# Kernel tuning notes

Measured on AMD Instinct MI355X. Metric: run time of the kernel, lower is better.

## Reference

```python
import jax, jax.numpy as jnp
import numpy as np

DIM = 1024
DT_RANK = 64
D_STATE = 16
B, L = 4, 512


def _layer_norm(x, gamma, beta, eps=1e-6):
    mu = jnp.mean(x, axis=-1, keepdims=True)
    var = jnp.mean(jnp.square(x - mu), axis=-1, keepdims=True)
    return (x - mu) * jax.lax.rsqrt(var + eps) * gamma + beta


def _ssm(u, W_x, b_x, W_dt, b_dt, A_log, Dp):
    # u: [b, l, d]  (d = dim_inner)
    r = W_dt.shape[0]
    n = A_log.shape[1]
    A = -jnp.exp(A_log)                                   # [d, n]
    dbc = u @ W_x + b_x                                   # [b, l, r + 2n]
    delta = jax.nn.softplus(dbc[..., :r] @ W_dt + b_dt)   # [b, l, d]
    Bmat = dbc[..., r:r + n]                              # [b, l, n]
    Cmat = dbc[..., r + n:]                               # [b, l, n]
    dA = jnp.exp(jnp.einsum('bld,dn->bldn', delta, A))    # [b, l, d, n]
    dBu = jnp.einsum('bld,bln,bld->bldn', delta, Bmat, u) # [b, l, d, n]

    def step(h, xs):
        dA_t, dBu_t, C_t = xs
        h = dA_t * h + dBu_t                              # [b, d, n]
        y = jnp.einsum('bdn,bn->bd', h, C_t)
        return h, y

    h0 = jnp.zeros((u.shape[0], u.shape[2], n), u.dtype)
    _, ys = jax.lax.scan(
        step, h0,
        (jnp.swapaxes(dA, 0, 1), jnp.swapaxes(dBu, 0, 1), jnp.swapaxes(Cmat, 0, 1)))
    y = jnp.swapaxes(ys, 0, 1)                            # [b, l, d]
    return y + u * Dp


def setup_inputs() -> dict:
    key = jax.random.key(0)
    ks = jax.random.split(key, 16)
    s = 0.02
    d, r, n = DIM, DT_RANK, D_STATE
    inp = {
        'inputs': jax.random.normal(ks[0], (B, L, d), jnp.float32),
        'gamma': jnp.ones((d,), jnp.float32),
        'beta': jnp.zeros((d,), jnp.float32),
        'W_proj': jax.random.normal(ks[1], (d, d), jnp.float32) * s,
        'b_proj': jnp.zeros((d,), jnp.float32),
        'W_fc': jax.random.normal(ks[2], (d, d), jnp.float32) * s,
        'b_fc': jnp.zeros((d,), jnp.float32),
        'W_bc': jax.random.normal(ks[3], (d, d), jnp.float32) * s,
        'b_bc': jnp.zeros((d,), jnp.float32),
        'W_x1': jax.random.normal(ks[4], (d, r + 2 * n), jnp.float32) * s,
        'b_x1': jnp.zeros((r + 2 * n,), jnp.float32),
        'W_dt1': jax.random.normal(ks[5], (r, d), jnp.float32) * s,
        'b_dt1': jnp.full((d,), -4.0, jnp.float32),
        'A_log1': jnp.log(jnp.broadcast_to(jnp.arange(1, n + 1, dtype=jnp.float32), (d, n))),
        'D1': jnp.ones((d,), jnp.float32),
        'W_x2': jax.random.normal(ks[6], (d, r + 2 * n), jnp.float32) * s,
        'b_x2': jnp.zeros((r + 2 * n,), jnp.float32),
        'W_dt2': jax.random.normal(ks[7], (r, d), jnp.float32) * s,
        'b_dt2': jnp.full((d,), -4.0, jnp.float32),
        'A_log2': jnp.log(jnp.broadcast_to(jnp.arange(1, n + 1, dtype=jnp.float32), (d, n))),
        'D2': jnp.ones((d,), jnp.float32),
    }
    return inp


def reference(inputs, gamma, beta, W_proj, b_proj, W_fc, b_fc, W_bc, b_bc,
              W_x1, b_x1, W_dt1, b_dt1, A_log1, D1,
              W_x2, b_x2, W_dt2, b_dt2, A_log2, D2):
    skip = inputs
    x = _layer_norm(inputs, gamma, beta)
    proj = x @ W_proj + b_proj           # same Dense called twice in original
    z = jax.nn.silu(proj)
    # forward direction: 1x1 conv (== dense) -> softplus -> SSM
    u1 = jax.nn.softplus(proj @ W_fc + b_fc)
    y1 = _ssm(u1, W_x1, b_x1, W_dt1, b_dt1, A_log1, D1)
    # backward direction branch (original does not flip the sequence)
    u2 = jax.nn.softplus(proj @ W_bc + b_bc)
    y2 = _ssm(u2, W_x2, b_x2, W_dt2, b_dt2, A_log2, D2)
    return y1 * z + y2 * z + skip
```

## Files before the change

### kernel.cpp

```cpp
#include <hip/hip_runtime.h>
#include <hip/hip_bf16.h>
#include <math.h>

#define DIM 1024
#define NTOK 2048
#define LSEQ 512
#define NB 4
#define DTR 64
#define DST 16
#define NCH 8
#define TCH 64

typedef unsigned short ushort_t;
typedef __attribute__((ext_vector_type(8))) short bf16x8;
typedef __attribute__((ext_vector_type(4))) float f32x4;

__device__ __forceinline__ float softplus_f(float x) {
    return (x > 20.f) ? x : log1pf(__expf(x));
}
__device__ __forceinline__ ushort_t to_bf16_bits(float f) {
    __hip_bfloat16 h = __float2bfloat16(f);
    return *(ushort_t*)&h;
}
__device__ __forceinline__ float bf16_bits_to_f(ushort_t b) {
    return __uint_as_float(((unsigned int)b) << 16);
}
template<int CTRL>
__device__ __forceinline__ float dpp_add(float x) {
    int xi = __float_as_int(x);
    int yi = __builtin_amdgcn_update_dpp(xi, xi, CTRL, 0xF, 0xF, false);
    return x + __int_as_float(yi);
}

__global__ __launch_bounds__(256) void wconv_kernel(
    const float* __restrict__ W0, const float* __restrict__ W1, const float* __restrict__ W2,
    ushort_t* __restrict__ T0, ushort_t* __restrict__ T1, ushort_t* __restrict__ T2) {
    const float* W = blockIdx.z == 0 ? W0 : blockIdx.z == 1 ? W1 : W2;
    ushort_t* T    = blockIdx.z == 0 ? T0 : blockIdx.z == 1 ? T1 : T2;
    __shared__ float tile[64][65];
    const int k0 = blockIdx.x * 64, n0 = blockIdx.y * 64;
    const int tid = threadIdx.x;
    #pragma unroll
    for (int p = 0; p < 16; ++p) {
        int idx = p * 256 + tid;
        int i = idx >> 6, j = idx & 63;
        tile[i][j] = W[(size_t)(k0 + i) * DIM + n0 + j];
    }
    __syncthreads();
    #pragma unroll
    for (int p = 0; p < 16; ++p) {
        int idx = p * 256 + tid;
        int j = idx >> 6, i = idx & 63;
        T[(size_t)(n0 + j) * DIM + k0 + i] = to_bf16_bits(tile[i][j]);
    }
}

__global__ __launch_bounds__(256) void ln_kernel(
    const float* __restrict__ x, const float* __restrict__ gamma,
    const float* __restrict__ beta, ushort_t* __restrict__ out) {
    const int row = blockIdx.x;
    const int tid = threadIdx.x;
    const float4* xr = (const float4*)(x + (size_t)row * DIM);
    float4 v = xr[tid];
    float s  = v.x + v.y + v.z + v.w;
    float sq = v.x*v.x + v.y*v.y + v.z*v.z + v.w*v.w;
    for (int o = 32; o > 0; o >>= 1) {
        s  += __shfl_down(s, o);
        sq += __shfl_down(sq, o);
    }
    __shared__ float red[8];
    if ((tid & 63) == 0) { red[tid >> 6] = s; red[4 + (tid >> 6)] = sq; }
    __syncthreads();
    float st  = red[0] + red[1] + red[2] + red[3];
    float sqt = red[4] + red[5] + red[6] + red[7];
    float mu = st * (1.f / DIM);
    float var = sqt * (1.f / DIM) - mu * mu;
    float rstd = rsqrtf(var + 1e-6f);
    float4 g = ((const float4*)gamma)[tid];
    float4 bt = ((const float4*)beta)[tid];
    ushort4 ob;
    ob.x = to_bf16_bits((v.x - mu) * rstd * g.x + bt.x);
    ob.y = to_bf16_bits((v.y - mu) * rstd * g.y + bt.y);
    ob.z = to_bf16_bits((v.z - mu) * rstd * g.z + bt.z);
    ob.w = to_bf16_bits((v.w - mu) * rstd * g.w + bt.w);
    ((ushort4*)(out + (size_t)row * DIM))[tid] = ob;
}

template<int ACT>
__global__ __launch_bounds__(256) void mfma_gemm(
    const ushort_t* __restrict__ A, const ushort_t* __restrict__ Bt,
    const float* __restrict__ bias, ushort_t* __restrict__ outb, float* __restrict__ outf) {
    __shared__ __align__(16) ushort_t Asl[2][64 * 64];
    __shared__ __align__(16) ushort_t Bsl[2][64 * 64];
    const int tid = threadIdx.x;
    const int bm = blockIdx.y * 64;
    const int bn = blockIdx.x * 64;
    const int lane = tid & 63;
    const int wid = tid >> 6;
    const int r  = lane & 15;
    const int kg = lane >> 4;
    const int wm = wid >> 1, wn = wid & 1;

    f32x4 acc[2][2] = {};

    auto STAGE = [&](int buf, int k0) {
        #pragma unroll
        for (int q = 0; q < 2; ++q) {
            int c = q * 256 + tid;
            int row = c >> 3;
            int ksl = ((c & 7) ^ (row & 7)) << 3;
            __builtin_amdgcn_global_load_lds(
                (const __attribute__((address_space(1))) void*)(A + (size_t)(bm + row) * DIM + k0 + ksl),
                (__attribute__((address_space(3))) void*)(&Asl[buf][c * 8]), 16, 0, 0);
        }
        #pragma unroll
        for (int q = 0; q < 2; ++q) {
            int c = q * 256 + tid;
            int row = c >> 3;
            int ksl = ((c & 7) ^ (row & 7)) << 3;
            __builtin_amdgcn_global_load_lds(
                (const __attribute__((address_space(1))) void*)(Bt + (size_t)(bn + row) * DIM + k0 + ksl),
                (__attribute__((address_space(3))) void*)(&Bsl[buf][c * 8]), 16, 0, 0);
        }
    };

    STAGE(0, 0);
    __syncthreads();
    int cur = 0;
    for (int t = 0; t < DIM / 64; ++t) {
        if (t + 1 < DIM / 64) STAGE(cur ^ 1, (t + 1) * 64);
        #pragma unroll
        for (int kk = 0; kk < 2; ++kk) {
            const int sw = ((kk * 4 + kg) ^ (r & 7)) << 3;
            bf16x8 af[2], bfr[2];
            #pragma unroll
            for (int mi = 0; mi < 2; ++mi)
                af[mi] = *(const bf16x8*)&Asl[cur][(wm * 32 + mi * 16 + r) * 64 + sw];
            #pragma unroll
            for (int nj = 0; nj < 2; ++nj)
                bfr[nj] = *(const bf16x8*)&Bsl[cur][(wn * 32 + nj * 16 + r) * 64 + sw];
            #pragma unroll
            for (int mi = 0; mi < 2; ++mi)
                #pragma unroll
                for (int nj = 0; nj < 2; ++nj)
                    acc[mi][nj] = __builtin_amdgcn_mfma_f32_16x16x32_bf16(af[mi], bfr[nj], acc[mi][nj], 0, 0, 0);
        }
        __syncthreads();
        cur ^= 1;
    }

    #pragma unroll
    for (int nj = 0; nj < 2; ++nj) {
        const int col = bn + wn * 32 + nj * 16 + r;
        const float bv = bias[col];
        #pragma unroll
        for (int mi = 0; mi < 2; ++mi) {
            const int rowb = bm + wm * 32 + mi * 16 + kg * 4;
            #pragma unroll
            for (int j = 0; j < 4; ++j) {
                float v = acc[mi][nj][j] + bv;
                size_t idx = (size_t)(rowb + j) * DIM + col;
                if (ACT == 0) {
                    outb[idx] = to_bf16_bits(v);
                    outf[idx] = v / (1.f + __expf(-v));
                } else {
                    outf[idx] = softplus_f(v);
                }
            }
        }
    }
}

__global__ __launch_bounds__(256) void dbc_kernel(
    const float* __restrict__ u1, const float* __restrict__ u2,
    const float* __restrict__ Wx1, const float* __restrict__ bx1,
    const float* __restrict__ Wx2, const float* __restrict__ bx2,
    float* __restrict__ dbc1, float* __restrict__ dbc2) {
    const int s = blockIdx.y;
    const float* __restrict__ u   = s ? u2   : u1;
    const float* __restrict__ Wx  = s ? Wx2  : Wx1;
    const float* __restrict__ bx  = s ? bx2  : bx1;
    float* __restrict__ dbc       = s ? dbc2 : dbc1;
    const int row0 = blockIdx.x * 8;
    const int tid = threadIdx.x;
    const int kh = tid >> 7;
    const int j  = tid & 127;
    __shared__ float part[8][96];
    float acc[8];
    if (j < 96) {
        const float bj = (kh == 0) ? bx[j] : 0.f;
        #pragma unroll
        for (int r = 0; r < 8; ++r) acc[r] = bj;
        const float* ur = u + (size_t)row0 * DIM + kh * 512;
        const float* wp = Wx + (size_t)(kh * 512) * 96 + j;
        for (int k = 0; k < 512; k += 4) {
            float4 uv[8];
            #pragma unroll
            for (int r = 0; r < 8; ++r) uv[r] = *(const float4*)(ur + (size_t)r * DIM + k);
            #pragma unroll
            for (int kk = 0; kk < 4; ++kk) {
                float w = wp[(size_t)(k + kk) * 96];
                #pragma unroll
                for (int r = 0; r < 8; ++r) {
                    float uvv = kk == 0 ? uv[r].x : kk == 1 ? uv[r].y : kk == 2 ? uv[r].z : uv[r].w;
                    acc[r] = fmaf(uvv, w, acc[r]);
                }
            }
        }
    }
    if (kh == 1 && j < 96) {
        #pragma unroll
        for (int r = 0; r < 8; ++r) part[r][j] = acc[r];
    }
    __syncthreads();
    if (kh == 0 && j < 96) {
        #pragma unroll
        for (int r = 0; r < 8; ++r)
            dbc[(size_t)(row0 + r) * 96 + j] = acc[r] + part[r][j];
    }
}

__global__ __launch_bounds__(256) void delta_kernel(
    const float* __restrict__ dbc1, const float* __restrict__ dbc2,
    const float* __restrict__ Wdt1, const float* __restrict__ bdt1,
    const float* __restrict__ Wdt2, const float* __restrict__ bdt2,
    ushort_t* __restrict__ delta1, ushort_t* __restrict__ delta2) {
    const int s = blockIdx.y;
    const float* __restrict__ dbc = s ? dbc2 : dbc1;
    const float* __restrict__ Wdt = s ? Wdt2 : Wdt1;
    const float* __restrict__ bdt = s ? bdt2 : bdt1;
    ushort_t* __restrict__ delta  = s ? delta2 : delta1;
    const int row0 = blockIdx.x * 4;
    const int tid = threadIdx.x;
    __shared__ float rs[4][64];
    rs[tid >> 6][tid & 63] = dbc[(size_t)(row0 + (tid >> 6)) * 96 + (tid & 63)];
    __syncthreads();
    float acc[4][4];
    #pragma unroll
    for (int i = 0; i < 4; ++i) {
        float b = bdt[tid + 256 * i];
        #pragma unroll
        for (int r = 0; r < 4; ++r) acc[r][i] = b;
    }
    for (int k = 0; k < 64; ++k) {
        #pragma unroll
        for (int i = 0; i < 4; ++i) {
            float w = Wdt[(size_t)k * DIM + tid + 256 * i];
            #pragma unroll
            for (int r = 0; r < 4; ++r) acc[r][i] = fmaf(rs[r][k], w, acc[r][i]);
        }
    }
    #pragma unroll
    for (int r = 0; r < 4; ++r)
        #pragma unroll
        for (int i = 0; i < 4; ++i)
            delta[(size_t)(row0 + r) * DIM + tid + 256 * i] = to_bf16_bits(softplus_f(acc[r][i]));
}

#define CH 4
#define SLOAD1(S, base) do { \
    _Pragma("unroll") for (int j_ = 0; j_ < CH; ++j_) { \
        const size_t rr_ = rowbase + (base) + j_; \
        dl##S[j_] = bf16_bits_to_f(delta[rr_ * DIM + d]); \
        uu##S[j_] = u[rr_ * DIM + d]; \
        Bn##S[j_] = dbc[rr_ * 96 + DTR + n]; \
    } \
} while (0)
#define SCOMP1(S) do { \
    _Pragma("unroll") for (int j_ = 0; j_ < CH; ++j_) { \
        float e_ = __expf(dl##S[j_] * a); \
        h = fmaf(e_, h, dl##S[j_] * Bn##S[j_] * uu##S[j_]); \
        sd += dl##S[j_]; \
    } \
} while (0)

__global__ __launch_bounds__(256) void scan_pass1(
    const ushort_t* __restrict__ delta1, const float* __restrict__ u1c, const float* __restrict__ dbc1,
    const float* __restrict__ Alog1,
    const ushort_t* __restrict__ delta2, const float* __restrict__ u2c, const float* __restrict__ dbc2,
    const float* __restrict__ Alog2,
    float* __restrict__ rbuf, float* __restrict__ sdbuf) {
    const int s = blockIdx.z;
    const ushort_t* __restrict__ delta = s ? delta2 : delta1;
    const float* __restrict__ u    = s ? u2c   : u1c;
    const float* __restrict__ dbc  = s ? dbc2  : dbc1;
    const float* __restrict__ Alog = s ? Alog2 : Alog1;
    const int tid = threadIdx.x;
    const int n = tid & 15;
    const int d = blockIdx.x * 16 + (tid >> 4);
    const int b = blockIdx.y >> 3;
    const int c = blockIdx.y & 7;
    const float a = -__expf(Alog[d * DST + n]);
    const size_t rowbase = (size_t)b * LSEQ + (size_t)c * TCH;
    float h = 0.f, sd = 0.f;
    float dlA[CH], uuA[CH], BnA[CH];
    float dlB[CH], uuB[CH], BnB[CH];
    SLOAD1(A, 0);
    for (int t = 0; t < TCH; t += 2 * CH) {
        SLOAD1(B, t + CH);
        SCOMP1(A);
        if (t + 2 * CH < TCH) SLOAD1(A, t + 2 * CH);
        SCOMP1(B);
    }
    const size_t ridx = ((((size_t)s * NB + b) * NCH + c) * DIM + d) * DST + n;
    rbuf[ridx] = h;
    if (n == 0) sdbuf[(((size_t)s * NB + b) * NCH + c) * DIM + d] = sd;
}

__global__ __launch_bounds__(256) void scan_combine(
    const float* __restrict__ Alog1, const float* __restrict__ Alog2,
    float* __restrict__ rbuf, const float* __restrict__ sdbuf) {
    const int tid = threadIdx.x;
    const int sb = blockIdx.x >> 6;
    const int s = sb >> 2, b = sb & 3;
    const int flat = (blockIdx.x & 63) * 256 + tid;
    const int d = flat >> 4, n = flat & 15;
    const float* Alog = s ? Alog2 : Alog1;
    const float a = -__expf(Alog[d * DST + n]);
    float hprev = 0.f;
    #pragma unroll
    for (int c = 0; c < NCH; ++c) {
        const size_t ridx = ((((size_t)s * NB + b) * NCH + c) * DIM + d) * DST + n;
        float rc = rbuf[ridx];
        float P = __expf(a * sdbuf[(((size_t)s * NB + b) * NCH + c) * DIM + d]);
        float hnew = fmaf(P, hprev, rc);
        rbuf[ridx] = hprev;
        hprev = hnew;
    }
}

#define SLOAD2(S, base) do { \
    _Pragma("unroll") for (int j_ = 0; j_ < CH; ++j_) { \
        const size_t rr_ = rowbase + (base) + j_; \
        dl##S[j_] = bf16_bits_to_f(delta[rr_ * DIM + d]); \
        uu##S[j_] = u[rr_ * DIM + d]; \
        Bn##S[j_] = dbc[rr_ * 96 + DTR + n]; \
        Cn##S[j_] = dbc[rr_ * 96 + DTR + DST + n]; \
    } \
} while (0)
#define SCOMP2(S, base) do { \
    _Pragma("unroll") for (int j_ = 0; j_ < CH; ++j_) { \
        float e_ = __expf(dl##S[j_] * a); \
        h = fmaf(e_, h, dl##S[j_] * Bn##S[j_] * uu##S[j_]); \
        float p_ = h * Cn##S[j_]; \
        p_ = dpp_add<0xB1>(p_); \
        p_ = dpp_add<0x4E>(p_); \
        p_ = dpp_add<0x124>(p_); \
        p_ = dpp_add<0x128>(p_); \
        if (n == 0) y[(rowbase + (base) + j_) * DIM + d] = fmaf(uu##S[j_], dcf, p_); \
    } \
} while (0)

__global__ __launch_bounds__(256) void scan_pass2(
    const ushort_t* __restrict__ delta1, const float* __restrict__ u1c, const float* __restrict__ dbc1,
    const float* __restrict__ Alog1, const float* __restrict__ D1p, float* __restrict__ y1,
    const ushort_t* __restrict__ delta2, const float* __restrict__ u2c, const float* __restrict__ dbc2,
    const float* __restrict__ Alog2, const float* __restrict__ D2p, float* __restrict__ y2,
    const float* __restrict__ rbuf) {
    const int s = blockIdx.z;
    const ushort_t* __restrict__ delta = s ? delta2 : delta1;
    const float* __restrict__ u    = s ? u2c   : u1c;
    const float* __restrict__ dbc  = s ? dbc2  : dbc1;
    const float* __restrict__ Alog = s ? Alog2 : Alog1;
    const float* __restrict__ Dp   = s ? D2p   : D1p;
    float* __restrict__ y          = s ? y2    : y1;
    const int tid = threadIdx.x;
    const int n = tid & 15;
    const int d = blockIdx.x * 16 + (tid >> 4);
    const int b = blockIdx.y >> 3;
    const int c = blockIdx.y & 7;
    const float a = -__expf(Alog[d * DST + n]);
    const float dcf = Dp[d];
    const size_t rowbase = (size_t)b * LSEQ + (size_t)c * TCH;
    float h = rbuf[((((size_t)s * NB + b) * NCH + c) * DIM + d) * DST + n];
    float dlA[CH], uuA[CH], BnA[CH], CnA[CH];
    float dlB[CH], uuB[CH], BnB[CH], CnB[CH];
    SLOAD2(A, 0);
    for (int t = 0; t < TCH; t += 2 * CH) {
        SLOAD2(B, t + CH);
        SCOMP2(A, t);
        if (t + 2 * CH < TCH) SLOAD2(A, t + 2 * CH);
        SCOMP2(B, t + CH);
    }
}

__global__ __launch_bounds__(256) void final_kernel(
    const float* __restrict__ y1, const float* __restrict__ y2,
    const float* __restrict__ skip, float* io) {
    const int i = blockIdx.x * 256 + threadIdx.x;
    float4 a = ((const float4*)y1)[i];
    float4 b = ((const float4*)y2)[i];
    float4 sk = ((const float4*)skip)[i];
    float4 z = ((float4*)io)[i];
    float4 o;
    o.x = (a.x + b.x) * z.x + sk.x;
    o.y = (a.y + b.y) * z.y + sk.y;
    o.z = (a.z + b.z) * z.z + sk.z;
    o.w = (a.w + b.w) * z.w + sk.w;
    ((float4*)io)[i] = o;
}

extern "C" void kernel_launch(void* const* d_in, const int* in_sizes, int n_in,
                              void* d_out, int out_size, void* d_ws, size_t ws_size,
                              hipStream_t stream) {
    const float* inputs = (const float*)d_in[0];
    const float* gamma  = (const float*)d_in[1];
    const float* beta   = (const float*)d_in[2];
    const float* W_proj = (const float*)d_in[3];
    const float* b_proj = (const float*)d_in[4];
    const float* W_fc   = (const float*)d_in[5];
    const float* b_fc   = (const float*)d_in[6];
    const float* W_bc   = (const float*)d_in[7];
    const float* b_bc   = (const float*)d_in[8];
    const float* W_x1   = (const float*)d_in[9];
    const float* b_x1   = (const float*)d_in[10];
    const float* W_dt1  = (const float*)d_in[11];
    const float* b_dt1  = (const float*)d_in[12];
    const float* A_log1 = (const float*)d_in[13];
    const float* D1     = (const float*)d_in[14];
    const float* W_x2   = (const float*)d_in[15];
    const float* b_x2   = (const float*)d_in[16];
    const float* W_dt2  = (const float*)d_in[17];
    const float* b_dt2  = (const float*)d_in[18];
    const float* A_log2 = (const float*)d_in[19];
    const float* D2     = (const float*)d_in[20];
    float* out = (float*)d_out;
    char* wsb  = (char*)d_ws;

    ushort_t* xln_bf  = (ushort_t*)wsb;
    ushort_t* proj_bf = (ushort_t*)(wsb + (4u << 20));
    float*    y1      = (float*)wsb;
    float*    u1      = (float*)(wsb + (8u << 20));
    float*    u2      = (float*)(wsb + (16u << 20));
    float*    y2      = (float*)(wsb + (24u << 20));
    ushort_t* delta1  = (ushort_t*)(wsb + (32u << 20));
    ushort_t* delta2  = (ushort_t*)(wsb + (36u << 20));
    ushort_t* WtP     = (ushort_t*)(wsb + (40u << 20));
    ushort_t* WtF     = (ushort_t*)(wsb + (42u << 20));
    ushort_t* WtB     = (ushort_t*)(wsb + (44u << 20));
    float*    rbuf    = (float*)(wsb + (40u << 20));
    float*    sdbuf   = (float*)(wsb + (44u << 20));
    float*    dbc1    = (float*)(wsb + (46u << 20));
    float*    dbc2    = dbc1 + (size_t)NTOK * 96;
    float*    zbuf    = out;

    wconv_kernel<<<dim3(16, 16, 3), 256, 0, stream>>>(W_proj, W_fc, W_bc, WtP, WtF, WtB);
    ln_kernel<<<NTOK, 256, 0, stream>>>(inputs, gamma, beta, xln_bf);
    mfma_gemm<0><<<dim3(DIM / 64, NTOK / 64), 256, 0, stream>>>(xln_bf, WtP, b_proj, proj_bf, zbuf);
    mfma_gemm<1><<<dim3(DIM / 64, NTOK / 64), 256, 0, stream>>>(proj_bf, WtF, b_fc, nullptr, u1);
    mfma_gemm<1><<<dim3(DIM / 64, NTOK / 64), 256, 0, stream>>>(proj_bf, WtB, b_bc, nullptr, u2);
    dbc_kernel<<<dim3(NTOK / 8, 2), 256, 0, stream>>>(u1, u2, W_x1, b_x1, W_x2, b_x2, dbc1, dbc2);
    delta_kernel<<<dim3(NTOK / 4, 2), 256, 0, stream>>>(dbc1, dbc2, W_dt1, b_dt1, W_dt2, b_dt2, delta1, delta2);
    scan_pass1<<<dim3(DIM / 16, NB * NCH, 2), 256, 0, stream>>>(delta1, u1, dbc1, A_log1,
                                                                delta2, u2, dbc2, A_log2, rbuf, sdbuf);
    scan_combine<<<512, 256, 0, stream>>>(A_log1, A_log2, rbuf, sdbuf);
    scan_pass2<<<dim3(DIM / 16, NB * NCH, 2), 256, 0, stream>>>(delta1, u1, dbc1, A_log1, D1, y1,
                                                                delta2, u2, dbc2, A_log2, D2, y2, rbuf);
    final_kernel<<<(size_t)NTOK * DIM / 4 / 256, 256, 0, stream>>>(y1, y2, inputs, out);
}
```

Measured before the change: 338.0 us.

## Fold dt projection into combined weight and compute delta via bf16 MFMA GEMM

Measured after the change: 313.7 us. -7.2%, faster.

```diff
diff --git a/kernel.cpp b/kernel.cpp
--- a/kernel.cpp
+++ b/kernel.cpp
@@ -163,98 +163,150 @@
                 if (ACT == 0) {
                     outb[idx] = to_bf16_bits(v);
                     outf[idx] = v / (1.f + __expf(-v));
+                } else if (ACT == 1) {
+                    float sp = softplus_f(v);
+                    outf[idx] = sp;
+                    outb[idx] = to_bf16_bits(sp);
                 } else {
-                    outf[idx] = softplus_f(v);
+                    outb[idx] = to_bf16_bits(softplus_f(v));
                 }
             }
         }
     }
 }
 
-__global__ __launch_bounds__(256) void dbc_kernel(
-    const float* __restrict__ u1, const float* __restrict__ u2,
-    const float* __restrict__ Wx1, const float* __restrict__ bx1,
-    const float* __restrict__ Wx2, const float* __restrict__ bx2,
-    float* __restrict__ dbc1, float* __restrict__ dbc2) {
-    const int s = blockIdx.y;
-    const float* __restrict__ u   = s ? u2   : u1;
+__global__ __launch_bounds__(256) void wcomb_kernel(
+    const float* __restrict__ Wx1, const float* __restrict__ Wdt1,
+    const float* __restrict__ bx1, const float* __restrict__ bdt1,
+    const float* __restrict__ Wx2, const float* __restrict__ Wdt2,
+    const float* __restrict__ bx2, const float* __restrict__ bdt2,
+    ushort_t* __restrict__ WcombT, ushort_t* __restrict__ WxBCt,
+    float* __restrict__ bcomb) {
+    const int s = blockIdx.z;
     const float* __restrict__ Wx  = s ? Wx2  : Wx1;
+    const float* __restrict__ Wdt = s ? Wdt2 : Wdt1;
     const float* __restrict__ bx  = s ? bx2  : bx1;
-    float* __restrict__ dbc       = s ? dbc2 : dbc1;
-    const int row0 = blockIdx.x * 8;
-    const int tid = threadIdx.x;
-    const int kh = tid >> 7;
-    const int j  = tid & 127;
-    __shared__ float part[8][96];
-    float acc[8];
-    if (j < 96) {
-        const float bj = (kh == 0) ? bx[j] : 0.f;
-        #pragma unroll
-        for (int r = 0; r < 8; ++r) acc[r] = bj;
-        const float* ur = u + (size_t)row0 * DIM + kh * 512;
-        const float* wp = Wx + (size_t)(kh * 512) * 96 + j;
-        for (int k = 0; k < 512; k += 4) {
-            float4 uv[8];
+    const float* __restrict__ bdt = s ? bdt2 : bdt1;
+    const int tid = threadIdx.x;
+    __shared__ float Xs[64][65];
+    __shared__ float Ds[64][65];
+    if (blockIdx.y == 16) {
+        const int i0 = blockIdx.x * 64;
+        #pragma unroll
+        for (int p = 0; p < 8; ++p) {
+            int idx = p * 256 + tid;
+            int c = idx >> 6, i = i0 + (idx & 63);
+            WxBCt[((size_t)s * 32 + c) * DIM + i] = to_bf16_bits(Wx[(size_t)i * 96 + 64 + c]);
+        }
+        if (tid < 64) {
+            int j = i0 + tid;
+            float acc = bdt[j];
+            for (int r = 0; r < 64; ++r) acc = fmaf(bx[r], Wdt[(size_t)r * DIM + j], acc);
+            bcomb[(size_t)s * DIM + j] = acc;
+        }
+        return;
+    }
+    const int i0 = blockIdx.x * 64, j0 = blockIdx.y * 64;
+    #pragma unroll
+    for (int p = 0; p < 16; ++p) {
+        int idx = p * 256 + tid;
+        int i = idx >> 6, r = idx & 63;
+        Xs[i][r] = Wx[(size_t)(i0 + i) * 96 + r];
+    }
+    #pragma unroll
+    for (int p = 0; p < 16; ++p) {
+        int idx = p * 256 + tid;
+        int r = idx >> 6, j = idx & 63;
+        Ds[r][j] = Wdt[(size_t)r * DIM + j0 + j];
+    }
+    __syncthreads();
+    const int tj = (tid >> 4) * 4, ti = (tid & 15) * 4;
+    float acc[4][4] = {};
+    for (int r = 0; r < 64; ++r) {
+        float a[4], b[4];
+        #pragma unroll
+        for (int q = 0; q < 4; ++q) a[q] = Ds[r][tj + q];
+        #pragma unroll
+        for (int q = 0; q < 4; ++q) b[q] = Xs[ti + q][r];
+        #pragma unroll
+        for (int ji = 0; ji < 4; ++ji)
             #pragma unroll
-            for (int r = 0; r < 8; ++r) uv[r] = *(const float4*)(ur + (size_t)r * DIM + k);
+            for (int ii = 0; ii < 4; ++ii)
+                acc[ji][ii] = fmaf(a[ji], b[ii], acc[ji][ii]);
+    }
+    #pragma unroll
+    for (int ji = 0; ji < 4; ++ji)
+        #pragma unroll
+        for (int ii = 0; ii < 4; ++ii)
+            WcombT[((size_t)s * DIM + j0 + tj + ji) * DIM + i0 + ti + ii] = to_bf16_bits(acc[ji][ii]);
+}
+
+__global__ __launch_bounds__(256) void bc_kernel(
+    const ushort_t* __restrict__ u1b, const ushort_t* __restrict__ u2b,
+    const ushort_t* __restrict__ WxBCt,
+    const float* __restrict__ bx1, const float* __restrict__ bx2,
+    float* __restrict__ BC) {
+    const int s = blockIdx.z;
+    const ushort_t* __restrict__ u  = s ? u2b : u1b;
+    const ushort_t* __restrict__ Bt = WxBCt + (size_t)s * 32 * DIM;
+    const float* __restrict__ bx    = s ? bx2 : bx1;
+    const int bm = blockIdx.x * 64;
+    const int kbase = blockIdx.y * 256;
+    __shared__ __align__(16) ushort_t Asl[2][64 * 64];
+    __shared__ __align__(16) ushort_t Bsl[2][32 * 64];
+    const int tid = threadIdx.x;
+    const int lane = tid & 63, wid = tid >> 6;
+    const int r = lane & 15, kg = lane >> 4;
+    f32x4 acc[2] = {};
+    auto STAGE = [&](int buf, int k0) {
+        #pragma unroll
+        for (int q = 0; q < 2; ++q) {
+            int c = q * 256 + tid;
+            int row = c >> 3;
+            int ksl = ((c & 7) ^ (row & 7)) << 3;
+            __builtin_amdgcn_global_load_lds(
+                (const __attribute__((address_space(1))) void*)(u + (size_t)(bm + row) * DIM + k0 + ksl),
+                (__attribute__((address_space(3))) void*)(&Asl[buf][c * 8]), 16, 0, 0);
+        }
+        {
+            int c = tid;
+            int row = c >> 3;
+            int ksl = ((c & 7) ^ (row & 7)) << 3;
+            __builtin_amdgcn_global_load_lds(
+                (const __attribute__((address_space(1))) void*)(Bt + (size_t)row * DIM + k0 + ksl),
+                (__attribute__((address_space(3))) void*)(&Bsl[buf][c * 8]), 16, 0, 0);
+        }
+    };
+    STAGE(0, kbase);
+    __syncthreads();
+    int cur = 0;
+    for (int t = 0; t < 4; ++t) {
+        if (t + 1 < 4) STAGE(cur ^ 1, kbase + (t + 1) * 64);
+        #pragma unroll
+        for (int kk = 0; kk < 2; ++kk) {
+            const int sw = ((kk * 4 + kg) ^ (r & 7)) << 3;
+            bf16x8 af = *(const bf16x8*)&Asl[cur][(wid * 16 + r) * 64 + sw];
             #pragma unroll
-            for (int kk = 0; kk < 4; ++kk) {
-                float w = wp[(size_t)(k + kk) * 96];
-                #pragma unroll
-                for (int r = 0; r < 8; ++r) {
-                    float uvv = kk == 0 ? uv[r].x : kk == 1 ? uv[r].y : kk == 2 ? uv[r].z : uv[r].w;
-                    acc[r] = fmaf(uvv, w, acc[r]);
-                }
+            for (int nj = 0; nj < 2; ++nj) {
+                bf16x8 bfr = *(const bf16x8*)&Bsl[cur][(nj * 16 + r) * 64 + sw];
+                acc[nj] = __builtin_amdgcn_mfma_f32_16x16x32_bf16(af, bfr, acc[nj], 0, 0, 0);
             }
         }
-    }
-    if (kh == 1 && j < 96) {
-        #pragma unroll
-        for (int r = 0; r < 8; ++r) part[r][j] = acc[r];
-    }
-    __syncthreads();
-    if (kh == 0 && j < 96) {
-        #pragma unroll
-        for (int r = 0; r < 8; ++r)
-            dbc[(size_t)(row0 + r) * 96 + j] = acc[r] + part[r][j];
-    }
-}
-
-__global__ __launch_bounds__(256) void delta_kernel(
-    const float* __restrict__ dbc1, const float* __restrict__ dbc2,
-    const float* __restrict__ Wdt1, const float* __restrict__ bdt1,
-    const float* __restrict__ Wdt2, const float* __restrict__ bdt2,
-    ushort_t* __restrict__ delta1, ushort_t* __restrict__ delta2) {
-    const int s = blockIdx.y;
-    const float* __restrict__ dbc = s ? dbc2 : dbc1;
-    const float* __restrict__ Wdt = s ? Wdt2 : Wdt1;
-    const float* __restrict__ bdt = s ? bdt2 : bdt1;
-    ushort_t* __restrict__ delta  = s ? delta2 : delta1;
-    const int row0 = blockIdx.x * 4;
-    const int tid = threadIdx.x;
-    __shared__ float rs[4][64];
-    rs[tid >> 6][tid & 63] = dbc[(size_t)(row0 + (tid >> 6)) * 96 + (tid & 63)];
-    __syncthreads();
-    float acc[4][4];
-    #pragma unroll
-    for (int i = 0; i < 4; ++i) {
-        float b = bdt[tid + 256 * i];
-        #pragma unroll
-        for (int r = 0; r < 4; ++r) acc[r][i] = b;
-    }
-    for (int k = 0; k < 64; ++k) {
-        #pragma unroll
-        for (int i = 0; i < 4; ++i) {
-            float w = Wdt[(size_t)k * DIM + tid + 256 * i];
-            #pragma unroll
-            for (int r = 0; r < 4; ++r) acc[r][i] = fmaf(rs[r][k], w, acc[r][i]);
-        }
-    }
-    #pragma unroll
-    for (int r = 0; r < 4; ++r)
-        #pragma unroll
-        for (int i = 0; i < 4; ++i)
-            delta[(size_t)(row0 + r) * DIM + tid + 256 * i] = to_bf16_bits(softplus_f(acc[r][i]));
+        __syncthreads();
+        cur ^= 1;
+    }
+    const bool kc0 = (blockIdx.y == 0);
+    #pragma unroll
+    for (int nj = 0; nj < 2; ++nj) {
+        const int col = nj * 16 + r;
+        #pragma unroll
+        for (int j = 0; j < 4; ++j) {
+            const int row = bm + wid * 16 + kg * 4 + j;
+            float v = acc[nj][j];
+            if (kc0) v += bx[64 + col];
+            atomicAdd(&BC[((size_t)s * NTOK + row) * 32 + col], v);
+        }
+    }
 }
 
 #define CH 4
@@ -263,7 +315,7 @@
         const size_t rr_ = rowbase + (base) + j_; \
         dl##S[j_] = bf16_bits_to_f(delta[rr_ * DIM + d]); \
         uu##S[j_] = u[rr_ * DIM + d]; \
-        Bn##S[j_] = dbc[rr_ * 96 + DTR + n]; \
+        Bn##S[j_] = BCp[rr_ * 32 + n]; \
     } \
 } while (0)
 #define SCOMP1(S) do { \
@@ -275,16 +327,16 @@
 } while (0)
 
 __global__ __launch_bounds__(256) void scan_pass1(
-    const ushort_t* __restrict__ delta1, const float* __restrict__ u1c, const float* __restrict__ dbc1,
+    const ushort_t* __restrict__ delta1, const float* __restrict__ u1c,
     const float* __restrict__ Alog1,
-    const ushort_t* __restrict__ delta2, const float* __restrict__ u2c, const float* __restrict__ dbc2,
-    const float* __restrict__ Alog2,
+    const ushort_t* __restrict__ delta2, const float* __restrict__ u2c,
+    const float* __restrict__ Alog2, const float* __restrict__ BC,
     float* __restrict__ rbuf, float* __restrict__ sdbuf) {
     const int s = blockIdx.z;
     const ushort_t* __restrict__ delta = s ? delta2 : delta1;
     const float* __restrict__ u    = s ? u2c   : u1c;
-    const float* __restrict__ dbc  = s ? dbc2  : dbc1;
     const float* __restrict__ Alog = s ? Alog2 : Alog1;
+    const float* __restrict__ BCp  = BC + (size_t)s * NTOK * 32;
     const int tid = threadIdx.x;
     const int n = tid & 15;
     const int d = blockIdx.x * 16 + (tid >> 4);
@@ -334,8 +386,8 @@
         const size_t rr_ = rowbase + (base) + j_; \
         dl##S[j_] = bf16_bits_to_f(delta[rr_ * DIM + d]); \
         uu##S[j_] = u[rr_ * DIM + d]; \
-        Bn##S[j_] = dbc[rr_ * 96 + DTR + n]; \
-        Cn##S[j_] = dbc[rr_ * 96 + DTR + DST + n]; \
+        Bn##S[j_] = BCp[rr_ * 32 + n]; \
+        Cn##S[j_] = BCp[rr_ * 32 + 16 + n]; \
     } \
 } while (0)
 #define SCOMP2(S, base) do { \
@@ -352,18 +404,18 @@
 } while (0)
 
 __global__ __launch_bounds__(256) void scan_pass2(
-    const ushort_t* __restrict__ delta1, const float* __restrict__ u1c, const float* __restrict__ dbc1,
+    const ushort_t* __restrict__ delta1, const float* __restrict__ u1c,
     const float* __restrict__ Alog1, const float* __restrict__ D1p, float* __restrict__ y1,
-    const ushort_t* __restrict__ delta2, const float* __restrict__ u2c, const float* __restrict__ dbc2,
+    const ushort_t* __restrict__ delta2, const float* __restrict__ u2c,
     const float* __restrict__ Alog2, const float* __restrict__ D2p, float* __restrict__ y2,
-    const float* __restrict__ rbuf) {
+    const float* __restrict__ BC, const float* __restrict__ rbuf) {
     const int s = blockIdx.z;
     const ushort_t* __restrict__ delta = s ? delta2 : delta1;
     const float* __restrict__ u    = s ? u2c   : u1c;
-    const float* __restrict__ dbc  = s ? dbc2  : dbc1;
     const float* __restrict__ Alog = s ? Alog2 : Alog1;
     const float* __restrict__ Dp   = s ? D2p   : D1p;
     float* __restrict__ y          = s ? y2    : y1;
+    const float* __restrict__ BCp  = BC + (size_t)s * NTOK * 32;
     const int tid = threadIdx.x;
     const int n = tid & 15;
     const int d = blockIdx.x * 16 + (tid >> 4);
@@ -432,29 +484,39 @@
     float*    y1      = (float*)wsb;
     float*    u1      = (float*)(wsb + (8u << 20));
     float*    u2      = (float*)(wsb + (16u << 20));
+    ushort_t* u1b     = (ushort_t*)(wsb + (24u << 20));
+    ushort_t* u2b     = (ushort_t*)(wsb + (28u << 20));
     float*    y2      = (float*)(wsb + (24u << 20));
     ushort_t* delta1  = (ushort_t*)(wsb + (32u << 20));
     ushort_t* delta2  = (ushort_t*)(wsb + (36u << 20));
     ushort_t* WtP     = (ushort_t*)(wsb + (40u << 20));
     ushort_t* WtF     = (ushort_t*)(wsb + (42u << 20));
     ushort_t* WtB     = (ushort_t*)(wsb + (44u << 20));
-    float*    rbuf    = (float*)(wsb + (40u << 20));
-    float*    sdbuf   = (float*)(wsb + (44u << 20));
-    float*    dbc1    = (float*)(wsb + (46u << 20));
-    float*    dbc2    = dbc1 + (size_t)NTOK * 96;
+    ushort_t* WxBCt   = (ushort_t*)(wsb + (40u << 20));
+    float*    bcomb   = (float*)(wsb + (41u << 20));
+    ushort_t* WcombT  = (ushort_t*)(wsb + (42u << 20));
+    float*    rbuf    = (float*)(wsb + (42u << 20));
+    float*    BC      = (float*)(wsb + (46u << 20));
+    float*    sdbuf   = (float*)(wsb + (46u << 20) + (512u << 10));
     float*    zbuf    = out;
 
     wconv_kernel<<<dim3(16, 16, 3), 256, 0, stream>>>(W_proj, W_fc, W_bc, WtP, WtF, WtB);
     ln_kernel<<<NTOK, 256, 0, stream>>>(inputs, gamma, beta, xln_bf);
     mfma_gemm<0><<<dim3(DIM / 64, NTOK / 64), 256, 0, stream>>>(xln_bf, WtP, b_proj, proj_bf, zbuf);
-    mfma_gemm<1><<<dim3(DIM / 64, NTOK / 64), 256, 0, stream>>>(proj_bf, WtF, b_fc, nullptr, u1);
-    mfma_gemm<1><<<dim3(DIM / 64, NTOK / 64), 256, 0, stream>>>(proj_bf, WtB, b_bc, nullptr, u2);
-    dbc_kernel<<<dim3(NTOK / 8, 2), 256, 0, stream>>>(u1, u2, W_x1, b_x1, W_x2, b_x2, dbc1, dbc2);
-    delta_kernel<<<dim3(NTOK / 4, 2), 256, 0, stream>>>(dbc1, dbc2, W_dt1, b_dt1, W_dt2, b_dt2, delta1, delta2);
-    scan_pass1<<<dim3(DIM / 16, NB * NCH, 2), 256, 0, stream>>>(delta1, u1, dbc1, A_log1,
-                                                                delta2, u2, dbc2, A_log2, rbuf, sdbuf);
+    mfma_gemm<1><<<dim3(DIM / 64, NTOK / 64), 256, 0, stream>>>(proj_bf, WtF, b_fc, u1b, u1);
+    mfma_gemm<1><<<dim3(DIM / 64, NTOK / 64), 256, 0, stream>>>(proj_bf, WtB, b_bc, u2b, u2);
+    wcomb_kernel<<<dim3(16, 17, 2), 256, 0, stream>>>(W_x1, W_dt1, b_x1, b_dt1,
+                                                      W_x2, W_dt2, b_x2, b_dt2,
+                                                      WcombT, WxBCt, bcomb);
+    hipMemsetAsync(BC, 0, (size_t)2 * NTOK * 32 * sizeof(float), stream);
+    bc_kernel<<<dim3(NTOK / 64, 4, 2), 256, 0, stream>>>(u1b, u2b, WxBCt, b_x1, b_x2, BC);
+    mfma_gemm<2><<<dim3(DIM / 64, NTOK / 64), 256, 0, stream>>>(u1b, WcombT, bcomb, delta1, nullptr);
+    mfma_gemm<2><<<dim3(DIM / 64, NTOK / 64), 256, 0, stream>>>(u2b, WcombT + (size_t)DIM * DIM,
+                                                                bcomb + DIM, delta2, nullptr);
+    scan_pass1<<<dim3(DIM / 16, NB * NCH, 2), 256, 0, stream>>>(delta1, u1, A_log1,
+                                                                delta2, u2, A_log2, BC, rbuf, sdbuf);
     scan_combine<<<512, 256, 0, stream>>>(A_log1, A_log2, rbuf, sdbuf);
-    scan_pass2<<<dim3(DIM / 16, NB * NCH, 2), 256, 0, stream>>>(delta1, u1, dbc1, A_log1, D1, y1,
-                                                                delta2, u2, dbc2, A_log2, D2, y2, rbuf);
+    scan_pass2<<<dim3(DIM / 16, NB * NCH, 2), 256, 0, stream>>>(delta1, u1, A_log1, D1, y1,
+                                                                delta2, u2, A_log2, D2, y2, BC, rbuf);
     final_kernel<<<(size_t)NTOK * DIM / 4 / 256, 256, 0, stream>>>(y1, y2, inputs, out);
 }
```
